# Performance work log

Hardware: AMD Instinct MI355X
Metric: run time of the kernel (lower is better)

## Reference

```python
import jax, jax.numpy as jnp
import numpy as np
from jax.scipy.special import logsumexp

S, B, T = 512, 1024, 48


def setup_inputs() -> dict:
    key = jax.random.key(0)
    k1, k2, k3, k4, k5 = jax.random.split(key, 5)
    return {
        "emissions": jax.random.normal(k1, (S, B, T), jnp.float32),
        "tags": jax.random.randint(k2, (S, B), 0, T, jnp.int32),
        "mask": jnp.ones((S, B), jnp.float32),
        "transitions": jax.random.normal(k3, (T, T), jnp.float32),
        "start_transitions": jax.random.normal(k4, (T,), jnp.float32),
        "stop_transitions": jax.random.normal(k5, (T,), jnp.float32),
    }


def _crf(emissions, tags, mask, transitions, start, stop):
    # emissions: (S,B,T), tags/mask: (S,B), time-major as in the torch module
    init = start[None, :] + emissions[0]  # (B,T)

    def step(carry, inp):
        fv, vv = carry  # forward (logsumexp) and viterbi (max) vars, each (B,T)
        em, m = inp  # (B,T), (B,)
        # scores[b, next, prev] = prev_var + transitions[prev,next] swapped to match
        # torch: forward_var.unsqueeze(1) + emission.unsqueeze(2) + transitions.unsqueeze(0)
        sc_f = fv[:, None, :] + transitions[None, :, :] + em[:, :, None]  # (B,T,T)
        sc_v = vv[:, None, :] + transitions[None, :, :] + em[:, :, None]
        new_fv = logsumexp(sc_f, axis=2)
        new_vv = jnp.max(sc_v, axis=2)
        m_ = m[:, None]
        fv = m_ * new_fv + (1.0 - m_) * fv
        vv = m_ * new_vv + (1.0 - m_) * vv
        return (fv, vv), None

    (fv, vv), _ = jax.lax.scan(step, (init, init), (emissions[1:], mask[1:]))
    alpha = logsumexp(fv + stop[None, :], axis=1)  # total_score (B,)
    best_path_score = jnp.max(vv + stop[None, :], axis=1)  # (B,)

    # real (gold) path score, fully vectorized over time
    em_tag = jnp.take_along_axis(emissions, tags[:, :, None].astype(jnp.int32), axis=2)[:, :, 0]  # (S,B)
    trans_sc = transitions[tags[:-1], tags[1:]]  # (S-1,B)
    real = (start[tags[0]]
            + jnp.sum(mask[1:] * (trans_sc + em_tag[1:]), axis=0)
            + stop[tags[-1]])
    loss = jnp.mean(alpha - real)
    return loss, real, alpha, best_path_score


def reference(emissions, tags, mask, transitions, start_transitions, stop_transitions):
    # Training-mode forward (return_best_path=False -> best_path is None in torch)
    return _crf(emissions, tags, mask, transitions, start_transitions, stop_transitions)
```

## Files before the change

### kernel.cpp

```cpp
#include <hip/hip_runtime.h>

#define S_LEN 512
#define B_DIM 1024
#define T_DIM 48
#define NPAIR 24
#define L2E 1.4426950408889634f
#define LN2 0.6931471805599453f

#define EXP2F(x) __builtin_amdgcn_exp2f(x)
#define LOG2F(x) __builtin_amdgcn_logf(x)

typedef _Float16 h2 __attribute__((ext_vector_type(2)));
typedef __fp16   r2 __attribute__((ext_vector_type(2)));

__device__ __forceinline__ h2 pkrtz(float a, float b) {
  r2 t = __builtin_amdgcn_cvt_pkrtz(a, b);
  return __builtin_bit_cast(h2, t);
}

__device__ __forceinline__ h2 bpick(h2 src, int lane) {
  int s = __builtin_amdgcn_readlane(__builtin_bit_cast(int, src), lane);
  return __builtin_bit_cast(h2, s);
}

template <int CTRL, int RMASK>
__device__ __forceinline__ float dppmovf(float v) {
  return __int_as_float(__builtin_amdgcn_update_dpp(
      __float_as_int(v), __float_as_int(v), CTRL, RMASK, 0xF, false));
}
template <int CTRL, int RMASK>
__device__ __forceinline__ float dppmaxf(float m) {
  return fmaxf(m, dppmovf<CTRL, RMASK>(m));
}
template <int CTRL, int RMASK>
__device__ __forceinline__ float dppaddf(float m) {
  return m + dppmovf<CTRL, RMASK>(m);
}

__device__ __forceinline__ float wave_max63(float m) {
  m = dppmaxf<0xB1, 0xF>(m);
  m = dppmaxf<0x4E, 0xF>(m);
  m = dppmaxf<0x141, 0xF>(m);
  m = dppmaxf<0x140, 0xF>(m);
  m = dppmaxf<0x142, 0xA>(m);
  m = dppmaxf<0x143, 0xC>(m);
  return __int_as_float(__builtin_amdgcn_readlane(__float_as_int(m), 63));
}
__device__ __forceinline__ float wave_sum63(float m) {
  m = dppaddf<0xB1, 0xF>(m);
  m = dppaddf<0x4E, 0xF>(m);
  m = dppaddf<0x141, 0xF>(m);
  m = dppaddf<0x140, 0xF>(m);
  m = dppaddf<0x142, 0xA>(m);
  m = dppaddf<0x143, 0xC>(m);
  return __int_as_float(__builtin_amdgcn_readlane(__float_as_int(m), 63));
}

__global__ __launch_bounds__(64)
void crf_scan(const float* __restrict__ em, const float* __restrict__ mask,
              const float* __restrict__ trans, const float* __restrict__ startT,
              const float* __restrict__ stopT, float* __restrict__ out)
{
  const int b    = blockIdx.x & (B_DIM - 1);
  const int mode = blockIdx.x >> 10;
  const int i    = threadIdx.x;
  const int ri   = (i < T_DIM) ? i : (T_DIM - 1);

  float v   = startT[ri] + em[(size_t)b * T_DIM + ri];
  float OFF = 0.f;

  const float* emb = em + (size_t)b * T_DIM + ri;
  const size_t estep = (size_t)B_DIM * T_DIM;
  float e1 = emb[1 * estep];
  float e2 = emb[2 * estep];
  float e3 = emb[3 * estep];
  float mk = mask[B_DIM + b];

  if (mode == 0) {
    h2 Epk[NPAIR];
#pragma unroll
    for (int k = 0; k < NPAIR; ++k)
      Epk[k] = pkrtz(EXP2F(trans[ri * T_DIM + 2 * k]     * L2E),
                     EXP2F(trans[ri * T_DIM + 2 * k + 1] * L2E));

    for (int s = 1; s < S_LEN; ++s) {
      int sp = (s + 3 < S_LEN) ? s + 3 : S_LEN - 1;
      float ep  = emb[(size_t)sp * estep];
      int sn = (s + 1 < S_LEN) ? s + 1 : S_LEN - 1;
      float mkn = mask[sn * B_DIM + b];

      float mf = wave_max63(v);
      float p  = EXP2F((v - mf) * L2E);
      h2 pp = pkrtz(p, dppmovf<0xB1, 0xF>(p));

      h2 a0{}, a1{}, a2{}, a3{};
#pragma unroll
      for (int k = 0; k < 6; ++k) {
        a0 += bpick(pp, 2 * k)        * Epk[k];
        a1 += bpick(pp, 2 * (k + 6))  * Epk[k + 6];
        a2 += bpick(pp, 2 * (k + 12)) * Epk[k + 12];
        a3 += bpick(pp, 2 * (k + 18)) * Epk[k + 18];
      }
      a0 += a1; a2 += a3; a0 += a2;
      float accF = (float)a0.x + (float)a0.y;

      float fnew = fmaf(LN2, LOG2F(fmaxf(accF, 1e-30f)), e1);
      float fold = v - mf;
      v = fmaf(mk, fnew - fold, fold);
      OFF += mf;

      e1 = e2; e2 = e3; e3 = ep; mk = mkn;
    }
    float q  = v + stopT[ri];
    float mq = wave_max63(q);
    float e  = EXP2F((q - mq) * L2E);
    e = (i < T_DIM) ? e : 0.f;
    float alpha = OFF + mq + LN2 * LOG2F(wave_sum63(e));
    if (i == 0) out[1 + B_DIM + b] = alpha;
  } else {
    h2 Tpk[NPAIR];
#pragma unroll
    for (int k = 0; k < NPAIR; ++k)
      Tpk[k] = pkrtz(trans[ri * T_DIM + 2 * k], trans[ri * T_DIM + 2 * k + 1]);

    const h2 NEG = {(_Float16)-60000.f, (_Float16)-60000.f};
    for (int s = 1; s < S_LEN; ++s) {
      int sp = (s + 3 < S_LEN) ? s + 3 : S_LEN - 1;
      float ep  = emb[(size_t)sp * estep];
      int sn = (s + 1 < S_LEN) ? s + 1 : S_LEN - 1;
      float mkn = mask[sn * B_DIM + b];

      float mv = wave_max63(v);
      float vr = v - mv;
      h2 vp = pkrtz(vr, dppmovf<0xB1, 0xF>(vr));

      h2 m0 = NEG, m1 = NEG;
#pragma unroll
      for (int k = 0; k < 12; ++k) {
        m0 = __builtin_elementwise_max(m0, bpick(vp, 2 * k)        + Tpk[k]);
        m1 = __builtin_elementwise_max(m1, bpick(vp, 2 * (k + 12)) + Tpk[k + 12]);
      }
      m0 = __builtin_elementwise_max(m0, m1);
      float mx = fmaxf((float)m0.x, (float)m0.y);

      float vnew = e1 + mx;
      float vold = v - mv;
      v = fmaf(mk, vnew - vold, vold);
      OFF += mv;

      e1 = e2; e2 = e3; e3 = ep; mk = mkn;
    }
    float best = OFF + wave_max63(v + stopT[ri]);
    if (i == 0) out[1 + 2 * B_DIM + b] = best;
  }
}

__global__ __launch_bounds__(256)
void crf_real(const float* __restrict__ em, const int* __restrict__ tags,
              const float* __restrict__ mask, const float* __restrict__ trans,
              const float* __restrict__ startT, const float* __restrict__ stopT,
              float* __restrict__ out)
{
  __shared__ float red[256];
  const int b = blockIdx.x;
  const int t = threadIdx.x;
  float acc = 0.f;
  for (int s = 1 + t; s < S_LEN; s += 256) {
    int   tp  = tags[(s - 1) * B_DIM + b];
    int   tc  = tags[s * B_DIM + b];
    float mkv = mask[s * B_DIM + b];
    float emt = em[((size_t)s * B_DIM + b) * T_DIM + tc];
    acc = fmaf(mkv, trans[tp * T_DIM + tc] + emt, acc);
  }
  red[t] = acc;
  __syncthreads();
  for (int w = 128; w > 0; w >>= 1) {
    if (t < w) red[t] += red[t + w];
    __syncthreads();
  }
  if (t == 0)
    out[1 + b] = startT[tags[b]] + stopT[tags[(S_LEN - 1) * B_DIM + b]] + red[0];
}

__global__ __launch_bounds__(256)
void crf_loss(float* __restrict__ out)
{
  __shared__ float red[256];
  int t = threadIdx.x;
  float a = 0.f;
  for (int b = t; b < B_DIM; b += 256)
    a += out[1 + B_DIM + b] - out[1 + b];
  red[t] = a;
  __syncthreads();
  for (int w = 128; w > 0; w >>= 1) {
    if (t < w) red[t] += red[t + w];
    __syncthreads();
  }
  if (t == 0) out[0] = red[0] * (1.0f / B_DIM);
}

extern "C" void kernel_launch(void* const* d_in, const int* in_sizes, int n_in,
                              void* d_out, int out_size, void* d_ws, size_t ws_size,
                              hipStream_t stream) {
  (void)in_sizes; (void)n_in; (void)d_ws; (void)ws_size; (void)out_size;
  const float* em     = (const float*)d_in[0];
  const int*   tags   = (const int*)d_in[1];
  const float* mask   = (const float*)d_in[2];
  const float* trans  = (const float*)d_in[3];
  const float* startT = (const float*)d_in[4];
  const float* stopT  = (const float*)d_in[5];
  float* out = (float*)d_out;

  hipLaunchKernelGGL(crf_scan, dim3(2 * B_DIM), dim3(64), 0, stream,
                     em, mask, trans, startT, stopT, out);
  hipLaunchKernelGGL(crf_real, dim3(B_DIM), dim3(256), 0, stream,
                     em, tags, mask, trans, startT, stopT, out);
  hipLaunchKernelGGL(crf_loss, dim3(1), dim3(256), 0, stream, out);
}
```

Measured before the change: 235.8 us.

## Broadcast previous-state vector via LDS float4 reads instead of fp16 readlane

Both recurrences now publish each step's state vector to a double-buffered shared-memory array and read it back as float4 broadcasts. This replaces 24 scalar readlane picks of packed fp16 pairs per step, along with their SGPR round-trips, with 12 LDS vector loads and plain fp32 FMAs or max operations. The Viterbi path also drops the per-step wave max normalization and the running offset, and the forward path folds its max into the log term. In exchange each step now needs a barrier and LDS latency, and the larger fp32 coefficient arrays raise register pressure.

```diff
diff --git a/kernel.cpp b/kernel.cpp
--- a/kernel.cpp
+++ b/kernel.cpp
@@ -3,25 +3,11 @@
 #define S_LEN 512
 #define B_DIM 1024
 #define T_DIM 48
-#define NPAIR 24
 #define L2E 1.4426950408889634f
 #define LN2 0.6931471805599453f
 
 #define EXP2F(x) __builtin_amdgcn_exp2f(x)
 #define LOG2F(x) __builtin_amdgcn_logf(x)
-
-typedef _Float16 h2 __attribute__((ext_vector_type(2)));
-typedef __fp16   r2 __attribute__((ext_vector_type(2)));
-
-__device__ __forceinline__ h2 pkrtz(float a, float b) {
-  r2 t = __builtin_amdgcn_cvt_pkrtz(a, b);
-  return __builtin_bit_cast(h2, t);
-}
-
-__device__ __forceinline__ h2 bpick(h2 src, int lane) {
-  int s = __builtin_amdgcn_readlane(__builtin_bit_cast(int, src), lane);
-  return __builtin_bit_cast(h2, s);
-}
 
 template <int CTRL, int RMASK>
 __device__ __forceinline__ float dppmovf(float v) {
@@ -61,13 +47,14 @@
               const float* __restrict__ trans, const float* __restrict__ startT,
               const float* __restrict__ stopT, float* __restrict__ out)
 {
+  __shared__ __align__(16) float Pbuf[2][64];
+
   const int b    = blockIdx.x & (B_DIM - 1);
   const int mode = blockIdx.x >> 10;
   const int i    = threadIdx.x;
   const int ri   = (i < T_DIM) ? i : (T_DIM - 1);
 
-  float v   = startT[ri] + em[(size_t)b * T_DIM + ri];
-  float OFF = 0.f;
+  float v = startT[ri] + em[(size_t)b * T_DIM + ri];
 
   const float* emb = em + (size_t)b * T_DIM + ri;
   const size_t estep = (size_t)B_DIM * T_DIM;
@@ -77,11 +64,10 @@
   float mk = mask[B_DIM + b];
 
   if (mode == 0) {
-    h2 Epk[NPAIR];
-#pragma unroll
-    for (int k = 0; k < NPAIR; ++k)
-      Epk[k] = pkrtz(EXP2F(trans[ri * T_DIM + 2 * k]     * L2E),
-                     EXP2F(trans[ri * T_DIM + 2 * k + 1] * L2E));
+    float Ef[T_DIM];
+#pragma unroll
+    for (int k = 0; k < T_DIM; ++k)
+      Ef[k] = EXP2F(trans[ri * T_DIM + k] * L2E);
 
     for (int s = 1; s < S_LEN; ++s) {
       int sp = (s + 3 < S_LEN) ? s + 3 : S_LEN - 1;
@@ -91,23 +77,23 @@
 
       float mf = wave_max63(v);
       float p  = EXP2F((v - mf) * L2E);
-      h2 pp = pkrtz(p, dppmovf<0xB1, 0xF>(p));
-
-      h2 a0{}, a1{}, a2{}, a3{};
-#pragma unroll
-      for (int k = 0; k < 6; ++k) {
-        a0 += bpick(pp, 2 * k)        * Epk[k];
-        a1 += bpick(pp, 2 * (k + 6))  * Epk[k + 6];
-        a2 += bpick(pp, 2 * (k + 12)) * Epk[k + 12];
-        a3 += bpick(pp, 2 * (k + 18)) * Epk[k + 18];
+      Pbuf[s & 1][i] = p;
+      __syncthreads();
+      const float4* lds4 = (const float4*)Pbuf[s & 1];
+
+      float a0 = 0.f, a1 = 0.f, a2 = 0.f, a3 = 0.f;
+#pragma unroll
+      for (int k = 0; k < 12; ++k) {
+        float4 q = lds4[k];
+        a0 = fmaf(q.x, Ef[4 * k + 0], a0);
+        a1 = fmaf(q.y, Ef[4 * k + 1], a1);
+        a2 = fmaf(q.z, Ef[4 * k + 2], a2);
+        a3 = fmaf(q.w, Ef[4 * k + 3], a3);
       }
-      a0 += a1; a2 += a3; a0 += a2;
-      float accF = (float)a0.x + (float)a0.y;
-
-      float fnew = fmaf(LN2, LOG2F(fmaxf(accF, 1e-30f)), e1);
-      float fold = v - mf;
-      v = fmaf(mk, fnew - fold, fold);
-      OFF += mf;
+      float accF = (a0 + a1) + (a2 + a3);
+
+      float fnew = fmaf(LN2, LOG2F(fmaxf(accF, 1e-30f)), e1 + mf);
+      v = fmaf(mk, fnew - v, v);
 
       e1 = e2; e2 = e3; e3 = ep; mk = mkn;
     }
@@ -115,42 +101,41 @@
     float mq = wave_max63(q);
     float e  = EXP2F((q - mq) * L2E);
     e = (i < T_DIM) ? e : 0.f;
-    float alpha = OFF + mq + LN2 * LOG2F(wave_sum63(e));
+    float alpha = mq + LN2 * LOG2F(wave_sum63(e));
     if (i == 0) out[1 + B_DIM + b] = alpha;
   } else {
-    h2 Tpk[NPAIR];
-#pragma unroll
-    for (int k = 0; k < NPAIR; ++k)
-      Tpk[k] = pkrtz(trans[ri * T_DIM + 2 * k], trans[ri * T_DIM + 2 * k + 1]);
-
-    const h2 NEG = {(_Float16)-60000.f, (_Float16)-60000.f};
+    float Tf[T_DIM];
+#pragma unroll
+    for (int k = 0; k < T_DIM; ++k)
+      Tf[k] = trans[ri * T_DIM + k];
+
     for (int s = 1; s < S_LEN; ++s) {
       int sp = (s + 3 < S_LEN) ? s + 3 : S_LEN - 1;
       float ep  = emb[(size_t)sp * estep];
       int sn = (s + 1 < S_LEN) ? s + 1 : S_LEN - 1;
       float mkn = mask[sn * B_DIM + b];
 
-      float mv = wave_max63(v);
-      float vr = v - mv;
-      h2 vp = pkrtz(vr, dppmovf<0xB1, 0xF>(vr));
-
-      h2 m0 = NEG, m1 = NEG;
+      Pbuf[s & 1][i] = v;
+      __syncthreads();
+      const float4* lds4 = (const float4*)Pbuf[s & 1];
+
+      float m0 = -3.0e38f, m1 = -3.0e38f, m2 = -3.0e38f, m3 = -3.0e38f;
 #pragma unroll
       for (int k = 0; k < 12; ++k) {
-        m0 = __builtin_elementwise_max(m0, bpick(vp, 2 * k)        + Tpk[k]);
-        m1 = __builtin_elementwise_max(m1, bpick(vp, 2 * (k + 12)) + Tpk[k + 12]);
+        float4 q = lds4[k];
+        m0 = fmaxf(m0, q.x + Tf[4 * k + 0]);
+        m1 = fmaxf(m1, q.y + Tf[4 * k + 1]);
+        m2 = fmaxf(m2, q.z + Tf[4 * k + 2]);
+        m3 = fmaxf(m3, q.w + Tf[4 * k + 3]);
       }
-      m0 = __builtin_elementwise_max(m0, m1);
-      float mx = fmaxf((float)m0.x, (float)m0.y);
+      float mx = fmaxf(fmaxf(m0, m1), fmaxf(m2, m3));
 
       float vnew = e1 + mx;
-      float vold = v - mv;
-      v = fmaf(mk, vnew - vold, vold);
-      OFF += mv;
+      v = fmaf(mk, vnew - v, v);
 
       e1 = e2; e2 = e3; e3 = ep; mk = mkn;
     }
-    float best = OFF + wave_max63(v + stopT[ri]);
+    float best = wave_max63(v + stopT[ri]);
     if (i == 0) out[1 + 2 * B_DIM + b] = best;
   }
 }
```

After: 267.1 us. +13.3%, slower.
